# Kernel tuning notes

Hardware: AMD Instinct MI355X
Metric: run time of the kernel (lower is better)

## Reference

```python
import jax, jax.numpy as jnp
import numpy as np
from jax import lax

T, B, S, D = 16, 8, 256, 1024
M, H = 1024, 8
HD = M // H
TAU_MEM = 0.99
TAU_GATE = 0.9
VTH = 1.0
LN_EPS = 1e-5


def lif(inp, tau, vth):
    """LIF over leading time axis. inp: (T, N, M). Returns (spikes, membrane trace)."""
    def step(v, i):
        v = tau * v + i                      # integrate with leak
        s = (v >= vth).astype(i.dtype)       # hard threshold spike
        return v - s * vth, (s, v)           # subtract reset; trace is pre-reset membrane
    v0 = jnp.zeros(inp.shape[1:], inp.dtype)
    _, (spikes, mv) = lax.scan(step, v0, inp)
    return spikes, mv


def setup_inputs() -> dict:
    key = jax.random.key(0)
    ks = jax.random.split(key, 6)
    inp = {
        "x": jax.random.normal(ks[0], (T, B, S, D), dtype=jnp.float32),
        "W_to_memory": jax.random.normal(ks[1], (M, D), dtype=jnp.float32) / np.sqrt(D),
        "W_gate": jax.random.normal(ks[2], (M, D), dtype=jnp.float32) / np.sqrt(D),
        "W_read_key": jax.random.normal(ks[3], (M, M), dtype=jnp.float32) / np.sqrt(M),
        "W_from_memory": jax.random.normal(ks[4], (D, M), dtype=jnp.float32) / np.sqrt(M),
        "read_query": jax.random.normal(ks[5], (H, HD), dtype=jnp.float32) * 0.02,
        "gate_threshold": jnp.float32(0.5),
        "ln_gamma": jnp.ones((D,), jnp.float32),
        "ln_beta": jnp.zeros((D,), jnp.float32),
        "memory_mix": jnp.float32(0.1),
    }
    return inp


def reference(x, W_to_memory, W_gate, W_read_key, W_from_memory, read_query,
              gate_threshold, ln_gamma, ln_beta, memory_mix):
    N = B * S
    xf = x.reshape(T, N, D)

    # memory write path
    mi = jnp.einsum('tnd,md->tnm', xf, W_to_memory)        # (T,N,M)
    ms, mv = lif(mi, TAU_MEM, VTH)

    # spike-gated write
    gi = jnp.einsum('tnd,md->tnm', xf, W_gate)
    gs, _ = lif(gi, TAU_GATE, VTH)
    gate_sig = gs.mean(axis=0)                              # (N,M)
    gate_mask = jax.nn.sigmoid((gate_sig - gate_threshold) * 10.0)

    # multi-head temporal attention over T
    mvh = mv.reshape(T, N, H, HD)
    mk = jnp.einsum('tnm,km->tnk', mv, W_read_key).reshape(T, N, H, HD)
    scale = 1.0 / np.sqrt(HD)
    attn_s = jnp.einsum('tnhd,hd->tnh', mk, read_query) * scale
    attn_w = jax.nn.softmax(attn_s.astype(jnp.float32), axis=0).astype(mv.dtype)
    mem_read = jnp.einsum('tnhd,tnh->nhd', mvh, attn_w).reshape(N, M)
    mem_read = mem_read * gate_mask

    # project back, layernorm, residual mix
    mem_out = jnp.einsum('nm,dm->nd', mem_read, W_from_memory).astype(jnp.float32)
    mu = mem_out.mean(axis=-1, keepdims=True)
    var = mem_out.var(axis=-1, keepdims=True)
    mem_out = (mem_out - mu) * lax.rsqrt(var + LN_EPS) * ln_gamma + ln_beta
    mem_out = mem_out.astype(x.dtype)

    mix = jax.nn.sigmoid(memory_mix)
    x_enhanced = x + mix * mem_out.reshape(1, B, S, D)
    return x_enhanced
```

## Files before the change

### kernel.cpp

```cpp
#include <hip/hip_runtime.h>
#include <hip/hip_bf16.h>
#include <hip/hip_fp16.h>

#define TT 16
#define NN 2048
#define DD 1024
#define MM 1024
#define HH 8
#define ROWS 32768
#define JJ 2048

typedef _Float16 f16x8 __attribute__((ext_vector_type(8)));
typedef float f32x4 __attribute__((ext_vector_type(4)));

#define SB  __builtin_amdgcn_sched_barrier(0)
#define BAR __builtin_amdgcn_s_barrier()

__device__ __forceinline__ void gload16(const void* g, void* l) {
    __builtin_amdgcn_global_load_lds((const __attribute__((address_space(1))) void*)g,
                                     (__attribute__((address_space(3))) void*)l, 16, 0, 0);
}

__global__ __launch_bounds__(256) void pack_hi(const float* __restrict__ in,
                                               __half* __restrict__ hi, long n4) {
    long i = (long)blockIdx.x * 256 + threadIdx.x;
    if (i >= n4) return;
    float4 v = ((const float4*)in)[i];
    ushort4 H = { __half_as_ushort(__float2half(v.x)), __half_as_ushort(__float2half(v.y)),
                  __half_as_ushort(__float2half(v.z)), __half_as_ushort(__float2half(v.w)) };
    ((ushort4*)hi)[i] = H;
}

__global__ __launch_bounds__(256) void pack_hilo(const float* __restrict__ in,
                                                 __half* __restrict__ hi,
                                                 __half* __restrict__ lo, long n4) {
    long i = (long)blockIdx.x * 256 + threadIdx.x;
    if (i >= n4) return;
    float4 v = ((const float4*)in)[i];
    __half h0 = __float2half(v.x), h1 = __float2half(v.y);
    __half h2 = __float2half(v.z), h3 = __float2half(v.w);
    __half l0 = __float2half(v.x - __half2float(h0));
    __half l1 = __float2half(v.y - __half2float(h1));
    __half l2 = __float2half(v.z - __half2float(h2));
    __half l3 = __float2half(v.w - __half2float(h3));
    ushort4 H = { __half_as_ushort(h0), __half_as_ushort(h1), __half_as_ushort(h2), __half_as_ushort(h3) };
    ushort4 L = { __half_as_ushort(l0), __half_as_ushort(l1), __half_as_ushort(l2), __half_as_ushort(l3) };
    ((ushort4*)hi)[i] = H;
    ((ushort4*)lo)[i] = L;
}

__global__ __launch_bounds__(256) void pack_hilo_perm(const float* __restrict__ in,
                                                      __half* __restrict__ hi,
                                                      __half* __restrict__ lo) {
    long i = (long)blockIdx.x * 256 + threadIdx.x;
    int R   = (int)(i >> 8);
    int d4  = (int)(i & 255);
    int r   = R & 255, blk = R >> 8;
    int n_l = ((r >> 7) & 1) * 8 + ((r >> 6) & 1) * 4 + ((r >> 2) & 3);
    int t   = ((r >> 4) & 3) * 4 + (r & 3);
    int n_g = blk * 16 + n_l;
    long src = ((long)t * NN + n_g) * 256 + d4;
    float4 v = ((const float4*)in)[src];
    __half h0 = __float2half(v.x), h1 = __float2half(v.y);
    __half h2 = __float2half(v.z), h3 = __float2half(v.w);
    __half l0 = __float2half(v.x - __half2float(h0));
    __half l1 = __float2half(v.y - __half2float(h1));
    __half l2 = __float2half(v.z - __half2float(h2));
    __half l3 = __float2half(v.w - __half2float(h3));
    ushort4 H = { __half_as_ushort(h0), __half_as_ushort(h1), __half_as_ushort(h2), __half_as_ushort(h3) };
    ushort4 L = { __half_as_ushort(l0), __half_as_ushort(l1), __half_as_ushort(l2), __half_as_ushort(l3) };
    ((ushort4*)hi)[i] = H;
    ((ushort4*)lo)[i] = L;
}

__global__ __launch_bounds__(256) void compute_wq(const float* __restrict__ Wrk,
                                                  const float* __restrict__ q,
                                                  float* __restrict__ wq) {
    int m = blockIdx.x * 256 + threadIdx.x;
    int h = blockIdx.y;
    const float* qh = q + h * 128;
    const float* wr = Wrk + (size_t)h * 128 * MM + m;
    float acc = 0.f;
    for (int hd = 0; hd < 128; hd++) acc = fmaf(qh[hd], wr[(size_t)hd * MM], acc);
    wq[h * MM + m] = acc * 0.08838834764831845f;
}

__global__ __launch_bounds__(512, 2)
void gemm8p(const __half* __restrict__ Ahi, const __half* __restrict__ Alo,
            const __half* __restrict__ Bhi, const __half* __restrict__ Blo,
            __half* __restrict__ mv, float* __restrict__ gmask,
            const float* __restrict__ gate_thr)
{
    extern __shared__ __align__(16) char smem[];
    char* AHb = smem;
    char* ALb = smem + 32768;
    char* BHb = smem + 65536;
    char* BLb = smem + 98304;

    const int tid = threadIdx.x, lane = tid & 63, wave = tid >> 6;
    const int l15 = lane & 15, l4 = lane >> 4;
    const int wm = wave >> 2, wn = wave & 3;

    const int orig = blockIdx.x;
    const int wg   = (orig & 7) * 128 + (orig >> 3);
    const int rb   = (wg >> 3) * 256;
    const int cb   = (wg & 7) * 256;

    auto stageU = [&](const __half* src, int row0, char* dstbase, int par, int kt, int s) {
        int t   = s * 512 + tid;
        int row = t >> 2;
        int p   = t & 3;
        int kb  = (p ^ ((row >> 1) & 3)) * 16;
        const char* g = (const char*)(src + (size_t)(row0 + row) * 1024 + kt * 32) + kb;
        gload16(g, dstbase + par * 16384 + (size_t)(s * 512 + wave * 64) * 16);
    };
    auto rdT = [&](const char* base, int par, int row) -> f16x8 {
        int p = l4 ^ ((row >> 1) & 3);
        return *(const f16x8*)(base + par * 16384 + row * 64 + p * 16);
    };

    f32x4 acc[8][4] = {};
    const int NKT = 32;

    stageU(Ahi, rb, AHb, 0, 0, 0); stageU(Ahi, rb, AHb, 0, 0, 1);
    stageU(Alo, rb, ALb, 0, 0, 0); stageU(Alo, rb, ALb, 0, 0, 1);
    stageU(Bhi, cb, BHb, 0, 0, 0); stageU(Bhi, cb, BHb, 0, 0, 1);
    stageU(Blo, cb, BLb, 0, 0, 0); stageU(Blo, cb, BLb, 0, 0, 1);

    for (int kt = 0; kt < NKT; kt++) {
        const int p = kt & 1, pn = p ^ 1;
        const bool pre = (kt + 1 < NKT);
        f16x8 a[8], bh[4], bl[4];

        asm volatile("s_waitcnt vmcnt(0)" ::: "memory");
        SB; BAR;

        #pragma unroll
        for (int i = 0; i < 8; i++) a[i] = rdT(AHb, p, wm * 128 + i * 16 + l15);
        #pragma unroll
        for (int n = 0; n < 4; n++) bh[n] = rdT(BHb, p, wn * 64 + n * 16 + l15);
        if (pre) {
            stageU(Ahi, rb, AHb, pn, kt + 1, 0); stageU(Ahi, rb, AHb, pn, kt + 1, 1);
            stageU(Alo, rb, ALb, pn, kt + 1, 0); stageU(Alo, rb, ALb, pn, kt + 1, 1);
        }
        __builtin_amdgcn_s_setprio(1);
        #pragma unroll
        for (int i = 0; i < 8; i++)
            #pragma unroll
            for (int n = 0; n < 4; n++)
                acc[i][n] = __builtin_amdgcn_mfma_f32_16x16x32_f16(a[i], bh[n], acc[i][n], 0, 0, 0);
        __builtin_amdgcn_s_setprio(0);

        #pragma unroll
        for (int n = 0; n < 4; n++) bl[n] = rdT(BLb, p, wn * 64 + n * 16 + l15);
        if (pre) {
            stageU(Bhi, cb, BHb, pn, kt + 1, 0); stageU(Bhi, cb, BHb, pn, kt + 1, 1);
            stageU(Blo, cb, BLb, pn, kt + 1, 0); stageU(Blo, cb, BLb, pn, kt + 1, 1);
        }
        __builtin_amdgcn_s_setprio(1);
        #pragma unroll
        for (int i = 0; i < 8; i++)
            #pragma unroll
            for (int n = 0; n < 4; n++)
                acc[i][n] = __builtin_amdgcn_mfma_f32_16x16x32_f16(a[i], bl[n], acc[i][n], 0, 0, 0);
        __builtin_amdgcn_s_setprio(0);

        #pragma unroll
        for (int i = 0; i < 8; i++) a[i] = rdT(ALb, p, wm * 128 + i * 16 + l15);
        __builtin_amdgcn_s_setprio(1);
        #pragma unroll
        for (int i = 0; i < 8; i++)
            #pragma unroll
            for (int n = 0; n < 4; n++)
                acc[i][n] = __builtin_amdgcn_mfma_f32_16x16x32_f16(a[i], bh[n], acc[i][n], 0, 0, 0);
        __builtin_amdgcn_s_setprio(0);
    }

    asm volatile("s_waitcnt lgkmcnt(0) vmcnt(0)" ::: "memory");
    SB; BAR;

    const int n_g_base = rb >> 4;
    if (cb < 1024) {
        __half* mvs = (__half*)smem;
        #pragma unroll
        for (int i2 = 0; i2 < 2; i2++) {
            int n_l = wm * 8 + i2 * 4 + l4;
            #pragma unroll
            for (int nf = 0; nf < 4; nf++) {
                int col = wn * 64 + nf * 16 + l15;
                float v = 0.f;
                #pragma unroll
                for (int tt = 0; tt < 4; tt++)
                    #pragma unroll
                    for (int reg = 0; reg < 4; reg++) {
                        int t = tt * 4 + reg;
                        v = 0.99f * v + acc[i2 * 4 + tt][nf][reg];
                        mvs[(t * 16 + n_l) * 256 + col] = __float2half(v);
                        if (v >= 1.0f) v -= 1.0f;
                    }
            }
        }
        SB; BAR;
        #pragma unroll
        for (int j = 0; j < 16; j++) {
            int k = j * 512 + tid;
            int e = k * 8;
            int t   = e >> 12;
            int n_l = (e >> 8) & 15;
            int m   = e & 255;
            float4 val = *(const float4*)((const char*)smem + (size_t)k * 16);
            *(float4*)(mv + ((size_t)(t * NN + n_g_base + n_l) * MM + cb + m)) = val;
        }
    } else {
        float thr = gate_thr[0];
        #pragma unroll
        for (int i2 = 0; i2 < 2; i2++) {
            int n_l = wm * 8 + i2 * 4 + l4;
            #pragma unroll
            for (int nf = 0; nf < 4; nf++) {
                int col = wn * 64 + nf * 16 + l15;
                float v = 0.f, cnt = 0.f;
                #pragma unroll
                for (int tt = 0; tt < 4; tt++)
                    #pragma unroll
                    for (int reg = 0; reg < 4; reg++) {
                        v = 0.9f * v + acc[i2 * 4 + tt][nf][reg];
                        if (v >= 1.0f) { v -= 1.0f; cnt += 1.0f; }
                    }
                float gs = cnt * 0.0625f;
                gmask[(size_t)(n_g_base + n_l) * MM + (cb - 1024) + col] =
                    1.0f / (1.0f + expf(-10.0f * (gs - thr)));
            }
        }
    }
}

template<int TERMS>
__global__ __launch_bounds__(256, 2)
void gemm_f16(const __half* __restrict__ Ahi, const __half* __restrict__ Alo,
              const __half* __restrict__ Bhi, const __half* __restrict__ Blo,
              float* __restrict__ C, int K, int ldc, int ncb_log2)
{
    __shared__ __align__(16) __half lds[2][4][8][512];
    const int tid  = threadIdx.x;
    const int lane = tid & 63;
    const int wave = tid >> 6;
    const int l15  = lane & 15, l4 = lane >> 4;

    const int nwg  = gridDim.x;
    const int orig = blockIdx.x;
    const int wg   = (orig & 7) * (nwg >> 3) + (orig >> 3);
    const int rb = (wg >> ncb_log2) * 128;
    const int cb = (wg & ((1 << ncb_log2) - 1)) * 128;

    auto stage = [&](int buf, int ks) {
        const int k0 = ks * 32;
        #pragma unroll
        for (int qq = 0; qq < 2; qq++) {
            int g = wave * 2 + qq;
            size_t aoff = (size_t)(rb + g * 16 + l15) * K + (k0 + 8 * l4);
            gload16(Ahi + aoff, &lds[buf][0][g][0]);
            if constexpr (TERMS == 3) gload16(Alo + aoff, &lds[buf][1][g][0]);
            size_t boff = (size_t)(cb + g * 16 + l15) * K + (k0 + 8 * l4);
            gload16(Bhi + boff, &lds[buf][2][g][0]);
            if constexpr (TERMS == 3) gload16(Blo + boff, &lds[buf][3][g][0]);
        }
    };

    const int wave_r = (wave >> 1) * 64;
    const int wave_c = (wave & 1) * 64;
    const int ag0 = wave_r >> 4;
    const int bg0 = wave_c >> 4;

    f32x4 acc[4][4] = {};
    const int nks = K >> 5;
    stage(0, 0);
    int buf = 0;
    for (int ks = 0; ks < nks; ks++) {
        __syncthreads();
        if (ks + 1 < nks) stage(buf ^ 1, ks + 1);
        f16x8 ah[4], bh[4], al[4], bl[4];
        #pragma unroll
        for (int i = 0; i < 4; i++) {
            ah[i] = *(const f16x8*)&lds[buf][0][ag0 + i][lane * 8];
            bh[i] = *(const f16x8*)&lds[buf][2][bg0 + i][lane * 8];
            if constexpr (TERMS == 3) {
                al[i] = *(const f16x8*)&lds[buf][1][ag0 + i][lane * 8];
                bl[i] = *(const f16x8*)&lds[buf][3][bg0 + i][lane * 8];
            }
        }
        #pragma unroll
        for (int m = 0; m < 4; m++)
            #pragma unroll
            for (int n = 0; n < 4; n++) {
                acc[m][n] = __builtin_amdgcn_mfma_f32_16x16x32_f16(ah[m], bh[n], acc[m][n], 0, 0, 0);
                if constexpr (TERMS == 3) {
                    acc[m][n] = __builtin_amdgcn_mfma_f32_16x16x32_f16(ah[m], bl[n], acc[m][n], 0, 0, 0);
                    acc[m][n] = __builtin_amdgcn_mfma_f32_16x16x32_f16(al[m], bh[n], acc[m][n], 0, 0, 0);
                }
            }
        buf ^= 1;
    }
    #pragma unroll
    for (int m = 0; m < 4; m++)
        #pragma unroll
        for (int n = 0; n < 4; n++) {
            int r0 = rb + wave_r + m * 16 + l4 * 4;
            int c  = cb + wave_c + n * 16 + l15;
            #pragma unroll
            for (int reg = 0; reg < 4; reg++)
                C[(size_t)(r0 + reg) * ldc + c] = acc[m][n][reg];
        }
}

__global__ __launch_bounds__(256)
void attn_memread(const __half* __restrict__ mv, const float* __restrict__ wq,
                  const float* __restrict__ gmask, __half* __restrict__ mem_read)
{
    int n = blockIdx.x;
    __shared__ __align__(16) __half smv[TT][1032];
    __shared__ float sw[HH][TT];
    __shared__ float ssm[HH][TT];
    int tid = threadIdx.x;

    for (int t = 0; t < TT; t++) {
        const ushort4* src = (const ushort4*)(mv + ((size_t)t * NN + n) * MM);
        ((ushort4*)&smv[t][0])[tid] = src[tid];
    }
    __syncthreads();

    if (tid < 128) {
        int h = tid >> 4, t = tid & 15;
        const float* w = wq + h * MM;
        float acc = 0.f;
        for (int m = 0; m < MM; m += 2) {
            float2 v = __half22float2(*(const __half2*)&smv[t][m]);
            acc = fmaf(v.x, w[m], acc);
            acc = fmaf(v.y, w[m + 1], acc);
        }
        sw[h][t] = acc;
    }
    __syncthreads();
    if (tid < 8) {
        int h = tid;
        float mx = -1e30f;
        for (int t = 0; t < TT; t++) mx = fmaxf(mx, sw[h][t]);
        float s = 0.f;
        for (int t = 0; t < TT; t++) { float e = __expf(sw[h][t] - mx); ssm[h][t] = e; s += e; }
        float inv = 1.0f / s;
        for (int t = 0; t < TT; t++) ssm[h][t] *= inv;
    }
    __syncthreads();

    const float* gm = gmask + (size_t)n * MM;
    #pragma unroll
    for (int mm = 0; mm < 4; mm++) {
        int m = tid + mm * 256;
        int h = m >> 7;
        float acc = 0.f;
        #pragma unroll
        for (int t = 0; t < TT; t++) acc = fmaf(__half2float(smv[t][m]), ssm[h][t], acc);
        acc *= gm[m];
        mem_read[(size_t)n * MM + m] = __float2half(acc);
    }
}

__global__ __launch_bounds__(256)
void ln_add(const float* __restrict__ mem_out, const float* __restrict__ x,
            const float* __restrict__ gamma, const float* __restrict__ beta,
            const float* __restrict__ mmix, float* __restrict__ out)
{
    int n = blockIdx.x, tid = threadIdx.x;
    int lane = tid & 63, wave = tid >> 6;
    __shared__ float sred[10];
    float4 v = ((const float4*)(mem_out + (size_t)n * DD))[tid];
    float s  = v.x + v.y + v.z + v.w;
    float ss = v.x * v.x + v.y * v.y + v.z * v.z + v.w * v.w;
    #pragma unroll
    for (int o = 32; o > 0; o >>= 1) { s += __shfl_down(s, o, 64); ss += __shfl_down(ss, o, 64); }
    if (lane == 0) { sred[wave * 2] = s; sred[wave * 2 + 1] = ss; }
    __syncthreads();
    if (tid == 0) {
        float S = 0.f, SS = 0.f;
        for (int w = 0; w < 4; w++) { S += sred[w * 2]; SS += sred[w * 2 + 1]; }
        float mu = S * (1.0f / DD);
        float var = SS * (1.0f / DD) - mu * mu;
        sred[8] = mu;
        sred[9] = rsqrtf(var + 1e-5f);
    }
    __syncthreads();
    float mu = sred[8], rs = sred[9];
    float4 g = ((const float4*)gamma)[tid];
    float4 b = ((const float4*)beta)[tid];
    float4 nv;
    nv.x = (v.x - mu) * rs * g.x + b.x;
    nv.y = (v.y - mu) * rs * g.y + b.y;
    nv.z = (v.z - mu) * rs * g.z + b.z;
    nv.w = (v.w - mu) * rs * g.w + b.w;
    float mix = 1.0f / (1.0f + expf(-mmix[0]));
    for (int t = 0; t < TT; t++) {
        size_t off = ((size_t)t * NN + n) * DD;
        float4 xv = ((const float4*)(x + off))[tid];
        float4 o;
        o.x = xv.x + mix * nv.x;
        o.y = xv.y + mix * nv.y;
        o.z = xv.z + mix * nv.z;
        o.w = xv.w + mix * nv.w;
        ((float4*)(out + off))[tid] = o;
    }
}

__global__ void ws_sentinel(float* out) { out[0] = 12345.0f; }

extern "C" void kernel_launch(void* const* d_in, const int* in_sizes, int n_in,
                              void* d_out, int out_size, void* d_ws, size_t ws_size,
                              hipStream_t stream)
{
    const float* x     = (const float*)d_in[0];
    const float* Wto   = (const float*)d_in[1];
    const float* Wg    = (const float*)d_in[2];
    const float* Wrk   = (const float*)d_in[3];
    const float* Wfrom = (const float*)d_in[4];
    const float* q     = (const float*)d_in[5];
    const float* gthr  = (const float*)d_in[6];
    const float* gamma = (const float*)d_in[7];
    const float* beta  = (const float*)d_in[8];
    const float* mmix  = (const float*)d_in[9];
    float* out = (float*)d_out;

    char* w = (char*)d_ws;
    size_t off = 0;
    auto alloc = [&](size_t bytes) -> void* {
        void* p = w + off;
        off += (bytes + 255) & ~(size_t)255;
        return p;
    };
    __half* x_hi   = (__half*)alloc((size_t)ROWS * DD * 2);
    __half* x_lo   = (__half*)alloc((size_t)ROWS * DD * 2);
    __half* wc_hi  = (__half*)alloc((size_t)JJ * DD * 2);
    __half* wc_lo  = (__half*)alloc((size_t)JJ * DD * 2);
    __half* wf_hi  = (__half*)alloc((size_t)DD * MM * 2);
    float*  wq     = (float*) alloc((size_t)HH * MM * 4);
    __half* mv     = (__half*)alloc((size_t)TT * NN * MM * 2);
    float*  gmask  = (float*) alloc((size_t)NN * MM * 4);
    __half* m_read = (__half*)alloc((size_t)NN * MM * 2);
    float*  m_out  = (float*) alloc((size_t)NN * DD * 4);

    if (off > ws_size) {
        ws_sentinel<<<1, 1, 0, stream>>>(out);
        return;
    }

    hipFuncSetAttribute((const void*)gemm8p, hipFuncAttributeMaxDynamicSharedMemorySize, 131072);

    pack_hilo_perm<<<ROWS * DD / 4 / 256, 256, 0, stream>>>(x, x_hi, x_lo);
    pack_hilo<<<(MM * DD / 4 + 255) / 256, 256, 0, stream>>>(Wto, wc_hi, wc_lo, MM * DD / 4);
    pack_hilo<<<(MM * DD / 4 + 255) / 256, 256, 0, stream>>>(Wg, wc_hi + (size_t)MM * DD, wc_lo + (size_t)MM * DD, MM * DD / 4);
    pack_hi<<<(DD * MM / 4 + 255) / 256, 256, 0, stream>>>(Wfrom, wf_hi, DD * MM / 4);
    compute_wq<<<dim3(4, 8), 256, 0, stream>>>(Wrk, q, wq);

    gemm8p<<<(ROWS / 256) * (JJ / 256), 512, 131072, stream>>>(x_hi, x_lo, wc_hi, wc_lo, mv, gmask, gthr);

    attn_memread<<<NN, 256, 0, stream>>>(mv, wq, gmask, m_read);

    gemm_f16<1><<<(NN / 128) * (DD / 128), 256, 0, stream>>>(m_read, m_read, wf_hi, wf_hi, m_out, MM, DD, 3);

    ln_add<<<NN, 256, 0, stream>>>(m_out, x, gamma, beta, mmix, out);
}
```

Before: 506.0 us.

## Switch fused write/gate GEMM to 32x32x16 MFMA with matching row permutation

Replaces the 16x16x32 f16 MFMA tiles in the fused memory/gate GEMM with 32x32x16 MFMA, cutting the instruction count per k-step and the LDS fragment reads per FLOP. The input row permutation in pack_hilo_perm is changed so that each 32x32 accumulator's 16 output registers map to the 16 timesteps of one neuron. This lets the LIF scan run over a single accumulator in the epilogue. The risk is that the new permutation and the read swizzle must match the 32x32 output layout exactly, or results will be wrong.

```diff
diff --git a/kernel.cpp b/kernel.cpp
--- a/kernel.cpp
+++ b/kernel.cpp
@@ -12,6 +12,7 @@
 
 typedef _Float16 f16x8 __attribute__((ext_vector_type(8)));
 typedef float f32x4 __attribute__((ext_vector_type(4)));
+typedef float f32x16 __attribute__((ext_vector_type(16)));
 
 #define SB  __builtin_amdgcn_sched_barrier(0)
 #define BAR __builtin_amdgcn_s_barrier()
@@ -56,8 +57,8 @@
     int R   = (int)(i >> 8);
     int d4  = (int)(i & 255);
     int r   = R & 255, blk = R >> 8;
-    int n_l = ((r >> 7) & 1) * 8 + ((r >> 6) & 1) * 4 + ((r >> 2) & 3);
-    int t   = ((r >> 4) & 3) * 4 + (r & 3);
+    int t   = ((r >> 3) & 3) * 4 + (r & 3);
+    int n_l = ((r >> 7) & 1) * 8 + ((r >> 5) & 3) * 2 + ((r >> 2) & 1);
     int n_g = blk * 16 + n_l;
     long src = ((long)t * NN + n_g) * 256 + d4;
     float4 v = ((const float4*)in)[src];
@@ -98,7 +99,7 @@
     char* BLb = smem + 98304;
 
     const int tid = threadIdx.x, lane = tid & 63, wave = tid >> 6;
-    const int l15 = lane & 15, l4 = lane >> 4;
+    const int l31 = lane & 31, lh = lane >> 5;
     const int wm = wave >> 2, wn = wave & 3;
 
     const int orig = blockIdx.x;
@@ -114,12 +115,13 @@
         const char* g = (const char*)(src + (size_t)(row0 + row) * 1024 + kt * 32) + kb;
         gload16(g, dstbase + par * 16384 + (size_t)(s * 512 + wave * 64) * 16);
     };
-    auto rdT = [&](const char* base, int par, int row) -> f16x8 {
-        int p = l4 ^ ((row >> 1) & 3);
-        return *(const f16x8*)(base + par * 16384 + row * 64 + p * 16);
+    auto rdT32 = [&](const char* base, int par, int rowblk, int ks) -> f16x8 {
+        int row = rowblk + l31;
+        int s   = (2 * ks + lh) ^ ((row >> 1) & 3);
+        return *(const f16x8*)(base + par * 16384 + row * 64 + s * 16);
     };
 
-    f32x4 acc[8][4] = {};
+    f32x16 acc[4][2] = {};
     const int NKT = 32;
 
     stageU(Ahi, rb, AHb, 0, 0, 0); stageU(Ahi, rb, AHb, 0, 0, 1);
@@ -130,49 +132,67 @@
     for (int kt = 0; kt < NKT; kt++) {
         const int p = kt & 1, pn = p ^ 1;
         const bool pre = (kt + 1 < NKT);
-        f16x8 a[8], bh[4], bl[4];
+        f16x8 a[4][2], bh[2][2], bl[2][2];
 
         asm volatile("s_waitcnt vmcnt(0)" ::: "memory");
         SB; BAR;
 
         #pragma unroll
-        for (int i = 0; i < 8; i++) a[i] = rdT(AHb, p, wm * 128 + i * 16 + l15);
-        #pragma unroll
-        for (int n = 0; n < 4; n++) bh[n] = rdT(BHb, p, wn * 64 + n * 16 + l15);
+        for (int i = 0; i < 4; i++)
+            #pragma unroll
+            for (int ks = 0; ks < 2; ks++)
+                a[i][ks] = rdT32(AHb, p, wm * 128 + i * 32, ks);
+        #pragma unroll
+        for (int nf = 0; nf < 2; nf++)
+            #pragma unroll
+            for (int ks = 0; ks < 2; ks++)
+                bh[nf][ks] = rdT32(BHb, p, wn * 64 + nf * 32, ks);
         if (pre) {
             stageU(Ahi, rb, AHb, pn, kt + 1, 0); stageU(Ahi, rb, AHb, pn, kt + 1, 1);
             stageU(Alo, rb, ALb, pn, kt + 1, 0); stageU(Alo, rb, ALb, pn, kt + 1, 1);
         }
         __builtin_amdgcn_s_setprio(1);
         #pragma unroll
-        for (int i = 0; i < 8; i++)
-            #pragma unroll
-            for (int n = 0; n < 4; n++)
-                acc[i][n] = __builtin_amdgcn_mfma_f32_16x16x32_f16(a[i], bh[n], acc[i][n], 0, 0, 0);
+        for (int i = 0; i < 4; i++)
+            #pragma unroll
+            for (int nf = 0; nf < 2; nf++)
+                #pragma unroll
+                for (int ks = 0; ks < 2; ks++)
+                    acc[i][nf] = __builtin_amdgcn_mfma_f32_32x32x16_f16(a[i][ks], bh[nf][ks], acc[i][nf], 0, 0, 0);
         __builtin_amdgcn_s_setprio(0);
 
         #pragma unroll
-        for (int n = 0; n < 4; n++) bl[n] = rdT(BLb, p, wn * 64 + n * 16 + l15);
+        for (int nf = 0; nf < 2; nf++)
+            #pragma unroll
+            for (int ks = 0; ks < 2; ks++)
+                bl[nf][ks] = rdT32(BLb, p, wn * 64 + nf * 32, ks);
         if (pre) {
             stageU(Bhi, cb, BHb, pn, kt + 1, 0); stageU(Bhi, cb, BHb, pn, kt + 1, 1);
             stageU(Blo, cb, BLb, pn, kt + 1, 0); stageU(Blo, cb, BLb, pn, kt + 1, 1);
         }
         __builtin_amdgcn_s_setprio(1);
         #pragma unroll
-        for (int i = 0; i < 8; i++)
-            #pragma unroll
-            for (int n = 0; n < 4; n++)
-                acc[i][n] = __builtin_amdgcn_mfma_f32_16x16x32_f16(a[i], bl[n], acc[i][n], 0, 0, 0);
+        for (int i = 0; i < 4; i++)
+            #pragma unroll
+            for (int nf = 0; nf < 2; nf++)
+                #pragma unroll
+                for (int ks = 0; ks < 2; ks++)
+                    acc[i][nf] = __builtin_amdgcn_mfma_f32_32x32x16_f16(a[i][ks], bl[nf][ks], acc[i][nf], 0, 0, 0);
         __builtin_amdgcn_s_setprio(0);
 
         #pragma unroll
-        for (int i = 0; i < 8; i++) a[i] = rdT(ALb, p, wm * 128 + i * 16 + l15);
+        for (int i = 0; i < 4; i++)
+            #pragma unroll
+            for (int ks = 0; ks < 2; ks++)
+                a[i][ks] = rdT32(ALb, p, wm * 128 + i * 32, ks);
         __builtin_amdgcn_s_setprio(1);
         #pragma unroll
-        for (int i = 0; i < 8; i++)
-            #pragma unroll
-            for (int n = 0; n < 4; n++)
-                acc[i][n] = __builtin_amdgcn_mfma_f32_16x16x32_f16(a[i], bh[n], acc[i][n], 0, 0, 0);
+        for (int i = 0; i < 4; i++)
+            #pragma unroll
+            for (int nf = 0; nf < 2; nf++)
+                #pragma unroll
+                for (int ks = 0; ks < 2; ks++)
+                    acc[i][nf] = __builtin_amdgcn_mfma_f32_32x32x16_f16(a[i][ks], bh[nf][ks], acc[i][nf], 0, 0, 0);
         __builtin_amdgcn_s_setprio(0);
     }
 
@@ -183,21 +203,18 @@
     if (cb < 1024) {
         __half* mvs = (__half*)smem;
         #pragma unroll
-        for (int i2 = 0; i2 < 2; i2++) {
-            int n_l = wm * 8 + i2 * 4 + l4;
-            #pragma unroll
-            for (int nf = 0; nf < 4; nf++) {
-                int col = wn * 64 + nf * 16 + l15;
+        for (int i = 0; i < 4; i++) {
+            int n_l = wm * 8 + i * 2 + lh;
+            #pragma unroll
+            for (int nf = 0; nf < 2; nf++) {
+                int m_local = wn * 64 + nf * 32 + l31;
                 float v = 0.f;
                 #pragma unroll
-                for (int tt = 0; tt < 4; tt++)
-                    #pragma unroll
-                    for (int reg = 0; reg < 4; reg++) {
-                        int t = tt * 4 + reg;
-                        v = 0.99f * v + acc[i2 * 4 + tt][nf][reg];
-                        mvs[(t * 16 + n_l) * 256 + col] = __float2half(v);
-                        if (v >= 1.0f) v -= 1.0f;
-                    }
+                for (int reg = 0; reg < 16; reg++) {
+                    v = 0.99f * v + acc[i][nf][reg];
+                    mvs[(reg * 16 + n_l) * 256 + m_local] = __float2half(v);
+                    if (v >= 1.0f) v -= 1.0f;
+                }
             }
         }
         SB; BAR;
@@ -214,21 +231,19 @@
     } else {
         float thr = gate_thr[0];
         #pragma unroll
-        for (int i2 = 0; i2 < 2; i2++) {
-            int n_l = wm * 8 + i2 * 4 + l4;
-            #pragma unroll
-            for (int nf = 0; nf < 4; nf++) {
-                int col = wn * 64 + nf * 16 + l15;
+        for (int i = 0; i < 4; i++) {
+            int n_l = wm * 8 + i * 2 + lh;
+            #pragma unroll
+            for (int nf = 0; nf < 2; nf++) {
+                int m_local = wn * 64 + nf * 32 + l31;
                 float v = 0.f, cnt = 0.f;
                 #pragma unroll
-                for (int tt = 0; tt < 4; tt++)
-                    #pragma unroll
-                    for (int reg = 0; reg < 4; reg++) {
-                        v = 0.9f * v + acc[i2 * 4 + tt][nf][reg];
-                        if (v >= 1.0f) { v -= 1.0f; cnt += 1.0f; }
-                    }
+                for (int reg = 0; reg < 16; reg++) {
+                    v = 0.9f * v + acc[i][nf][reg];
+                    if (v >= 1.0f) { v -= 1.0f; cnt += 1.0f; }
+                }
                 float gs = cnt * 0.0625f;
-                gmask[(size_t)(n_g_base + n_l) * MM + (cb - 1024) + col] =
+                gmask[(size_t)(n_g_base + n_l) * MM + (cb - 1024) + m_local] =
                     1.0f / (1.0f + expf(-10.0f * (gs - thr)));
             }
         }
```

After: 552.6 us. 1.09x slower.

## Pack GEMM operands into pre-tiled LDS-image layout for contiguous staging

Applied to the files above, without the earlier changes.

The packing kernels now write the fp16 hi/lo operand splits in a tiled layout that matches the GEMM's shared-memory tile image: 256-row blocks by 32-wide k-slices, with k-chunks laid out as separate planes. The GEMM's global-to-LDS staging then becomes a fully contiguous 16-byte-per-thread copy, and the LDS reads drop the XOR swizzle in favour of a plane-strided address. The intent is more coalesced staging loads and simpler addressing in the main GEMM. The trade-off is that the pack kernels now have each thread read 64 contiguous floats from its own row, which coalesces less well, and the unswizzled LDS reads may cause bank conflicts.

```diff
diff --git a/kernel.cpp b/kernel.cpp
--- a/kernel.cpp
+++ b/kernel.cpp
@@ -12,6 +12,7 @@
 
 typedef _Float16 f16x8 __attribute__((ext_vector_type(8)));
 typedef float f32x4 __attribute__((ext_vector_type(4)));
+typedef unsigned short u16x8 __attribute__((ext_vector_type(8)));
 
 #define SB  __builtin_amdgcn_sched_barrier(0)
 #define BAR __builtin_amdgcn_s_barrier()
@@ -31,46 +32,42 @@
     ((ushort4*)hi)[i] = H;
 }
 
-__global__ __launch_bounds__(256) void pack_hilo(const float* __restrict__ in,
-                                                 __half* __restrict__ hi,
-                                                 __half* __restrict__ lo, long n4) {
-    long i = (long)blockIdx.x * 256 + threadIdx.x;
-    if (i >= n4) return;
-    float4 v = ((const float4*)in)[i];
-    __half h0 = __float2half(v.x), h1 = __float2half(v.y);
-    __half h2 = __float2half(v.z), h3 = __float2half(v.w);
-    __half l0 = __float2half(v.x - __half2float(h0));
-    __half l1 = __float2half(v.y - __half2float(h1));
-    __half l2 = __float2half(v.z - __half2float(h2));
-    __half l3 = __float2half(v.w - __half2float(h3));
-    ushort4 H = { __half_as_ushort(h0), __half_as_ushort(h1), __half_as_ushort(h2), __half_as_ushort(h3) };
-    ushort4 L = { __half_as_ushort(l0), __half_as_ushort(l1), __half_as_ushort(l2), __half_as_ushort(l3) };
-    ((ushort4*)hi)[i] = H;
-    ((ushort4*)lo)[i] = L;
-}
-
-__global__ __launch_bounds__(256) void pack_hilo_perm(const float* __restrict__ in,
-                                                      __half* __restrict__ hi,
-                                                      __half* __restrict__ lo) {
-    long i = (long)blockIdx.x * 256 + threadIdx.x;
-    int R   = (int)(i >> 8);
-    int d4  = (int)(i & 255);
-    int r   = R & 255, blk = R >> 8;
-    int n_l = ((r >> 7) & 1) * 8 + ((r >> 6) & 1) * 4 + ((r >> 2) & 3);
-    int t   = ((r >> 4) & 3) * 4 + (r & 3);
-    int n_g = blk * 16 + n_l;
-    long src = ((long)t * NN + n_g) * 256 + d4;
-    float4 v = ((const float4*)in)[src];
-    __half h0 = __float2half(v.x), h1 = __float2half(v.y);
-    __half h2 = __float2half(v.z), h3 = __float2half(v.w);
-    __half l0 = __float2half(v.x - __half2float(h0));
-    __half l1 = __float2half(v.y - __half2float(h1));
-    __half l2 = __float2half(v.z - __half2float(h2));
-    __half l3 = __float2half(v.w - __half2float(h3));
-    ushort4 H = { __half_as_ushort(h0), __half_as_ushort(h1), __half_as_ushort(h2), __half_as_ushort(h3) };
-    ushort4 L = { __half_as_ushort(l0), __half_as_ushort(l1), __half_as_ushort(l2), __half_as_ushort(l3) };
-    ((ushort4*)hi)[i] = H;
-    ((ushort4*)lo)[i] = L;
+template<bool PERM>
+__global__ __launch_bounds__(256)
+void pack_tiled(const float* __restrict__ in, __half* __restrict__ hi,
+                __half* __restrict__ lo) {
+    const int rblk = blockIdx.x >> 4;
+    const int kt2  = blockIdx.x & 15;
+    const int r    = threadIdx.x;
+    int src_row;
+    if (PERM) {
+        int t   = ((r >> 4) & 3) * 4 + (r & 3);
+        int n_l = ((r >> 7) & 1) * 8 + ((r >> 6) & 1) * 4 + ((r >> 2) & 3);
+        src_row = t * NN + rblk * 16 + n_l;
+    } else {
+        src_row = rblk * 256 + r;
+    }
+    const float4* s4 = (const float4*)(in + (size_t)src_row * 1024 + kt2 * 64);
+    float f[64];
+    #pragma unroll
+    for (int q = 0; q < 16; q++) {
+        float4 v = s4[q];
+        f[q * 4 + 0] = v.x; f[q * 4 + 1] = v.y; f[q * 4 + 2] = v.z; f[q * 4 + 3] = v.w;
+    }
+    #pragma unroll
+    for (int j = 0; j < 8; j++) {
+        u16x8 H, L;
+        #pragma unroll
+        for (int e = 0; e < 8; e++) {
+            float x = f[j * 8 + e];
+            __half h = __float2half(x);
+            H[e] = __half_as_ushort(h);
+            L[e] = __half_as_ushort(__float2half(x - __half2float(h)));
+        }
+        size_t off = ((size_t)(rblk * 32 + kt2 * 2 + (j >> 2))) * 8192 + (j & 3) * 2048 + r * 8;
+        *(u16x8*)(hi + off) = H;
+        *(u16x8*)(lo + off) = L;
+    }
 }
 
 __global__ __launch_bounds__(256) void compute_wq(const float* __restrict__ Wrk,
@@ -107,16 +104,12 @@
     const int cb   = (wg & 7) * 256;
 
     auto stageU = [&](const __half* src, int row0, char* dstbase, int par, int kt, int s) {
-        int t   = s * 512 + tid;
-        int row = t >> 2;
-        int p   = t & 3;
-        int kb  = (p ^ ((row >> 1) & 3)) * 16;
-        const char* g = (const char*)(src + (size_t)(row0 + row) * 1024 + kt * 32) + kb;
+        const char* g = (const char*)(src + (size_t)((row0 >> 8) * 32 + kt) * 8192)
+                        + (size_t)(s * 512 + tid) * 16;
         gload16(g, dstbase + par * 16384 + (size_t)(s * 512 + wave * 64) * 16);
     };
     auto rdT = [&](const char* base, int par, int row) -> f16x8 {
-        int p = l4 ^ ((row >> 1) & 3);
-        return *(const f16x8*)(base + par * 16384 + row * 64 + p * 16);
+        return *(const f16x8*)(base + par * 16384 + l4 * 4096 + row * 16);
     };
 
     f32x4 acc[8][4] = {};
@@ -453,9 +446,9 @@
 
     hipFuncSetAttribute((const void*)gemm8p, hipFuncAttributeMaxDynamicSharedMemorySize, 131072);
 
-    pack_hilo_perm<<<ROWS * DD / 4 / 256, 256, 0, stream>>>(x, x_hi, x_lo);
-    pack_hilo<<<(MM * DD / 4 + 255) / 256, 256, 0, stream>>>(Wto, wc_hi, wc_lo, MM * DD / 4);
-    pack_hilo<<<(MM * DD / 4 + 255) / 256, 256, 0, stream>>>(Wg, wc_hi + (size_t)MM * DD, wc_lo + (size_t)MM * DD, MM * DD / 4);
+    pack_tiled<true><<<(ROWS / 256) * 16, 256, 0, stream>>>(x, x_hi, x_lo);
+    pack_tiled<false><<<(MM / 256) * 16, 256, 0, stream>>>(Wto, wc_hi, wc_lo);
+    pack_tiled<false><<<(MM / 256) * 16, 256, 0, stream>>>(Wg, wc_hi + (size_t)MM * DD, wc_lo + (size_t)MM * DD);
     pack_hi<<<(DD * MM / 4 + 255) / 256, 256, 0, stream>>>(Wfrom, wf_hi, DD * MM / 4);
     compute_wq<<<dim3(4, 8), 256, 0, stream>>>(Wrk, q, wq);
 
```

Result: no change. 496.2 us (-1.9%).
